# Kernel tuning notes

Hardware: AMD Instinct MI355X
Metric: run time of the kernel (lower is better)

The kernel has to match this reference:

```python
import jax, jax.numpy as jnp
import numpy as np

N_NODES = 50000
N_EDGES = 800000
DIM_IN, DIM_H, DIM_OUT = 256, 128, 64  # hidden widths: 256 -> 128 -> 64, sage1 out = 2*DIM_H


def sage_conv(x, src, dst, Wl, bl, Wr):
    # PyG SAGEConv (mean aggr): out = lin_l(mean over incoming x_src) + lin_r(x)
    n = x.shape[0]
    agg = jax.ops.segment_sum(x[src], dst, num_segments=n)  # [N, F]
    deg = jax.ops.segment_sum(jnp.ones((src.shape[0],), x.dtype), dst, num_segments=n)
    mean = agg / jnp.maximum(deg, 1.0)[:, None]
    return mean @ Wl + bl + x @ Wr


def setup_inputs() -> dict:
    key = jax.random.key(0)
    ks = jax.random.split(key, 12)
    def lin(k, fan_in, fan_out):
        bound = 1.0 / np.sqrt(fan_in)
        return jax.random.uniform(k, (fan_in, fan_out), jnp.float32, -bound, bound)
    h1 = 2 * DIM_H  # 256
    return {
        "x": jax.random.normal(ks[0], (N_NODES, DIM_IN), jnp.float32),
        "edge_index": jax.random.randint(ks[1], (2, N_EDGES), 0, N_NODES, jnp.int64),
        "W1l": lin(ks[2], DIM_IN, h1), "b1": jnp.zeros((h1,), jnp.float32), "W1r": lin(ks[3], DIM_IN, h1),
        "W2l": lin(ks[4], h1, DIM_H), "b2": jnp.zeros((DIM_H,), jnp.float32), "W2r": lin(ks[5], h1, DIM_H),
        "W3l": lin(ks[6], DIM_H, DIM_OUT), "b3": jnp.zeros((DIM_OUT,), jnp.float32), "W3r": lin(ks[7], DIM_H, DIM_OUT),
    }


def reference(x, edge_index, W1l, b1, W1r, W2l, b2, W2r, W3l, b3, W3r):
    src, dst = edge_index[0], edge_index[1]
    h = jax.nn.relu(sage_conv(x, src, dst, W1l, b1, W1r))
    # dropout disabled (training=False)
    h = jax.nn.relu(sage_conv(h, src, dst, W2l, b2, W2r))
    h = sage_conv(h, src, dst, W3l, b3, W3r)
    return (h, jax.nn.log_softmax(h, axis=1))
```

## Files before the change

kernel.cpp:

```cpp
#include <hip/hip_runtime.h>
#include <hip/hip_bf16.h>

#define N_NODES 50000
#define N_EDGES 800000
#define MP 50048
#define NB 98
#define BSH 9
#define CAP 10240

typedef unsigned short ushort_t;
typedef unsigned int uint_t;
typedef __attribute__((ext_vector_type(8))) __bf16 bf16x8;
typedef __attribute__((ext_vector_type(4))) float f32x4;
typedef __attribute__((ext_vector_type(2))) float f32x2;

__device__ __forceinline__ float bf2f(uint_t u) {
    union { uint_t i; float f; } v; v.i = u << 16; return v.f;
}
__device__ __forceinline__ ushort_t f2bf(float f) {
    union { float f; uint_t i; } v; v.f = f;
    uint_t u = v.i;
    return (ushort_t)((u + 0x7FFFu + ((u >> 16) & 1u)) >> 16);
}
__device__ __forceinline__ void accf8(float* a, uint2 d) {
    f32x2 p;
    p = __builtin_amdgcn_cvt_pk_f32_fp8(d.x, false); a[0] += p.x; a[1] += p.y;
    p = __builtin_amdgcn_cvt_pk_f32_fp8(d.x, true);  a[2] += p.x; a[3] += p.y;
    p = __builtin_amdgcn_cvt_pk_f32_fp8(d.y, false); a[4] += p.x; a[5] += p.y;
    p = __builtin_amdgcn_cvt_pk_f32_fp8(d.y, true);  a[6] += p.x; a[7] += p.y;
}
__device__ __forceinline__ uint_t pk_hi(float a, float b) {
    return __builtin_amdgcn_perm(__float_as_uint(b), __float_as_uint(a), 0x07060302);
}

__device__ __forceinline__ void pack_one(const float* Wl, const float* Wr,
                                         ushort_t* P, int K, int F, int t) {
    int NOUT = 2 * F;
    int lane = t & 63;
    int frag = t >> 6;
    int nct = NOUT / 16;
    int ct = frag % nct;
    int kt = frag / nct;
    int col = ct * 16 + (lane & 15);
    const float* W = (col < F) ? Wl : Wr;
    int c = (col < F) ? col : col - F;
    int k0 = kt * 32 + (lane >> 4) * 8;
    uint_t w[4];
    #pragma unroll
    for (int p = 0; p < 4; ++p) {
        ushort_t lo = f2bf(W[(size_t)(k0 + 2 * p) * F + c]);
        ushort_t hi = f2bf(W[(size_t)(k0 + 2 * p + 1) * F + c]);
        w[p] = (uint_t)lo | ((uint_t)hi << 16);
    }
    *(reinterpret_cast<uint4*>(P) + t) = make_uint4(w[0], w[1], w[2], w[3]);
}

__global__ void pack_all_k(const float* __restrict__ W1l, const float* __restrict__ W1r,
                           const float* __restrict__ W2l, const float* __restrict__ W2r,
                           const float* __restrict__ W3l, const float* __restrict__ W3r,
                           ushort_t* __restrict__ pB1, ushort_t* __restrict__ pB2,
                           ushort_t* __restrict__ pB3, int* __restrict__ bcur) {
    int tid = blockIdx.x * 256 + threadIdx.x;
    if (tid < 16384)       pack_one(W1l, W1r, pB1, 256, 256, tid);
    else if (tid < 24576)  pack_one(W2l, W2r, pB2, 256, 128, tid - 16384);
    else if (tid < 26624)  pack_one(W3l, W3r, pB3, 128, 64, tid - 24576);
    else {
        int z = tid - 26624;
        if (z < NB) bcur[z] = z * CAP;
    }
}

__global__ __launch_bounds__(256) void binA_k(const int* __restrict__ src,
                                              const int* __restrict__ dst,
                                              int* __restrict__ bcur,
                                              uint_t* __restrict__ ebuf, int E) {
    __shared__ int cnt[NB];
    __shared__ int base[NB];
    int t = threadIdx.x;
    if (t < NB) cnt[t] = 0;
    __syncthreads();
    int myE = blockIdx.x * 2048 + t * 8;
    uint_t pk[8];
    int bk[8];
    int nval = 0;
    if (myE + 8 <= E) {
        int4 d0 = *reinterpret_cast<const int4*>(dst + myE);
        int4 d1 = *reinterpret_cast<const int4*>(dst + myE + 4);
        int4 s0 = *reinterpret_cast<const int4*>(src + myE);
        int4 s1 = *reinterpret_cast<const int4*>(src + myE + 4);
        int dd[8] = {d0.x, d0.y, d0.z, d0.w, d1.x, d1.y, d1.z, d1.w};
        int ss[8] = {s0.x, s0.y, s0.z, s0.w, s1.x, s1.y, s1.z, s1.w};
        nval = 8;
        #pragma unroll
        for (int i = 0; i < 8; ++i) {
            pk[i] = ((uint_t)dd[i] << 16) | (uint_t)ss[i];
            bk[i] = dd[i] >> BSH;
            atomicAdd(&cnt[bk[i]], 1);
        }
    } else {
        for (int e = myE; e < E && nval < 8; ++e) {
            int d = dst[e];
            pk[nval] = ((uint_t)d << 16) | (uint_t)src[e];
            bk[nval] = d >> BSH;
            atomicAdd(&cnt[bk[nval]], 1);
            ++nval;
        }
    }
    __syncthreads();
    if (t < NB) {
        int c = cnt[t];
        base[t] = c ? atomicAdd(&bcur[t], c) : 0;
        cnt[t] = 0;
    }
    __syncthreads();
    for (int i = 0; i < nval; ++i) {
        int r = atomicAdd(&cnt[bk[i]], 1);
        ebuf[base[bk[i]] + r] = pk[i];
    }
}

__global__ void scanB_k(const int* __restrict__ bcur, int* __restrict__ sOffs) {
    __shared__ int s[128];
    int t = threadIdx.x;
    int c = (t < NB) ? (bcur[t] - t * CAP) : 0;
    s[t] = c;
    __syncthreads();
    #pragma unroll
    for (int d = 1; d < 128; d <<= 1) {
        int v = (t >= d) ? s[t - d] : 0;
        __syncthreads();
        s[t] += v;
        __syncthreads();
    }
    if (t < NB) sOffs[t] = s[t] - c;
}

__global__ __launch_bounds__(256) void binB2_k(const uint_t* __restrict__ ebuf,
                                               const int* __restrict__ bcur,
                                               const int* __restrict__ sOffs,
                                               int* __restrict__ offs,
                                               ushort_t* __restrict__ csrc) {
    __shared__ uint_t eLDS[CAP];
    __shared__ int lhist[512];
    __shared__ int lpre[512];
    __shared__ ushort_t lsrc[CAP];
    int b = blockIdx.x;
    int t = threadIdx.x;
    int n0 = b << BSH;
    int cntE = bcur[b] - b * CAP;
    int obase = sOffs[b];

    for (int i = t; i < 512; i += 256) lhist[i] = 0;
    __syncthreads();
    for (int i = t; i < cntE; i += 256) {
        uint_t pk = ebuf[b * CAP + i];
        eLDS[i] = pk;
        atomicAdd(&lhist[(int)(pk >> 16) - n0], 1);
    }
    __syncthreads();
    int h0 = lhist[2 * t], h1 = lhist[2 * t + 1];
    int pairv = h0 + h1;
    lpre[t] = pairv;
    __syncthreads();
    #pragma unroll
    for (int d = 1; d < 256; d <<= 1) {
        int v = (t >= d) ? lpre[t - d] : 0;
        __syncthreads();
        lpre[t] += v;
        __syncthreads();
    }
    int excl = lpre[t] - pairv;
    __syncthreads();
    lpre[2 * t] = excl;
    lpre[2 * t + 1] = excl + h0;
    __syncthreads();
    for (int i = t; i < 512; i += 256) {
        int node = n0 + i;
        if (node < N_NODES) offs[node] = obase + lpre[i];
    }
    if (b == NB - 1 && t == 0) offs[N_NODES] = N_EDGES;
    for (int i = t; i < 512; i += 256) lhist[i] = lpre[i];
    __syncthreads();
    for (int i = t; i < cntE; i += 256) {
        uint_t pk = eLDS[i];
        int p = atomicAdd(&lhist[(int)(pk >> 16) - n0], 1);
        lsrc[p] = (ushort_t)(pk & 0xffffu);
    }
    __syncthreads();
    for (int i = t; i < cntE; i += 256) csrc[obase + i] = lsrc[i];
}

template <int K, int NOUT, int NCB, int PF, bool F32A, int BPG>
__global__ __launch_bounds__(256, 2) void gemm_k(
    const void* __restrict__ Av, const ushort_t* __restrict__ Bp,
    unsigned char* __restrict__ Pout, ushort_t* __restrict__ Rout, int nvalid) {
    constexpr int KT = K / 32;
    constexpr int CTW = NCB / 64;
    constexpr int NCG = NOUT / NCB;
    constexpr int RS = NOUT - PF;
    constexpr int PADE = K + 8;
    constexpr int NTILES = MP / 32;
    constexpr int NWR = K / 64;
    __shared__ ushort_t Atile[32 * PADE];

    int cg = (NCG > 1) ? ((int)blockIdx.x % NCG) : 0;
    int bid = (NCG > 1) ? ((int)blockIdx.x / NCG) : (int)blockIdx.x;
    int wave = threadIdx.x >> 6;
    int lane = threadIdx.x & 63;
    int ct0 = cg * (NCB / 16) + wave * CTW;

    bf16x8 breg[KT][CTW];
    #pragma unroll
    for (int kt = 0; kt < KT; ++kt)
        #pragma unroll
        for (int ct = 0; ct < CTW; ++ct)
            breg[kt][ct] = *reinterpret_cast<const bf16x8*>(
                Bp + ((size_t)(kt * (NOUT / 16) + ct0 + ct) * 64 + lane) * 8);

    int arowoff = lane & 15;
    int r0 = (lane >> 4) * 4;
    int srow = threadIdx.x >> 3;
    int sel = (threadIdx.x & 7) * (K / 8);

    for (int t = bid; t < NTILES; t += BPG) {
        int rowBase = t * 32;
        __syncthreads();
        {
            int grow = min(rowBase + srow, nvalid - 1);
            ushort_t* dst = &Atile[srow * PADE + sel];
            if (F32A) {
                const float* A = (const float*)Av + (size_t)grow * K + sel;
                #pragma unroll
                for (int i = 0; i < NWR; ++i) {
                    float4 f0 = *reinterpret_cast<const float4*>(A + i * 8);
                    float4 f1 = *reinterpret_cast<const float4*>(A + i * 8 + 4);
                    uint4 w;
                    w.x = pk_hi(f0.x, f0.y);
                    w.y = pk_hi(f0.z, f0.w);
                    w.z = pk_hi(f1.x, f1.y);
                    w.w = pk_hi(f1.z, f1.w);
                    *reinterpret_cast<uint4*>(dst + i * 8) = w;
                }
            } else {
                const ushort_t* A = (const ushort_t*)Av + (size_t)grow * K + sel;
                #pragma unroll
                for (int i = 0; i < NWR; ++i)
                    *reinterpret_cast<uint4*>(dst + i * 8) =
                        *reinterpret_cast<const uint4*>(A + i * 8);
            }
        }
        __syncthreads();

        f32x4 acc[2][CTW];
        #pragma unroll
        for (int r = 0; r < 2; ++r)
            #pragma unroll
            for (int c = 0; c < CTW; ++c) acc[r][c] = (f32x4){0.f, 0.f, 0.f, 0.f};

        const ushort_t* A0 = &Atile[arowoff * PADE + (lane >> 4) * 8];
        #pragma unroll
        for (int kt = 0; kt < KT; ++kt) {
            bf16x8 x0 = *reinterpret_cast<const bf16x8*>(A0 + kt * 32);
            bf16x8 x1 = *reinterpret_cast<const bf16x8*>(A0 + 16 * PADE + kt * 32);
            #pragma unroll
            for (int ct = 0; ct < CTW; ++ct) {
                acc[0][ct] = __builtin_amdgcn_mfma_f32_16x16x32_bf16(breg[kt][ct], x0, acc[0][ct], 0, 0, 0);
                acc[1][ct] = __builtin_amdgcn_mfma_f32_16x16x32_bf16(breg[kt][ct], x1, acc[1][ct], 0, 0, 0);
            }
        }

        #pragma unroll
        for (int r = 0; r < 2; ++r) {
            int xrow = rowBase + r * 16 + arowoff;
            #pragma unroll
            for (int ct = 0; ct < CTW; ++ct) {
                int wc = (ct0 + ct) * 16 + r0;
                f32x4 v = acc[r][ct];
                if (PF > 0 && wc < PF) {
                    uint_t u = __builtin_amdgcn_cvt_pk_fp8_f32(v[0], v[1], 0u, false);
                    u = __builtin_amdgcn_cvt_pk_fp8_f32(v[2], v[3], u, true);
                    *reinterpret_cast<uint_t*>(Pout + (size_t)xrow * PF + wc) = u;
                } else {
                    uint2 w;
                    w.x = (uint_t)f2bf(v[0]) | ((uint_t)f2bf(v[1]) << 16);
                    w.y = (uint_t)f2bf(v[2]) | ((uint_t)f2bf(v[3]) << 16);
                    *reinterpret_cast<uint2*>(Rout + (size_t)xrow * RS + (wc - PF)) = w;
                }
            }
        }
    }
}

template <int F, bool FINAL>
__global__ __launch_bounds__(256) void aggP8_k(
    const unsigned char* __restrict__ P, const int* __restrict__ offs,
    const ushort_t* __restrict__ csrc, const ushort_t* __restrict__ R,
    const float* __restrict__ bias, ushort_t* __restrict__ H,
    float* __restrict__ hout, float* __restrict__ lout, int n) {
    constexpr int LPG = F / 8;
    constexpr int G = 64 / LPG;
    constexpr int U = (G >= 4) ? 1 : (4 / G);
    constexpr int ST = G * U;
    int wid = (blockIdx.x * 256 + threadIdx.x) >> 6;
    int lane = threadIdx.x & 63;
    int g = lane / LPG;
    int sub = lane & (LPG - 1);
    int colbase = sub * 8;
    int n0 = 2 * wid, n1 = 2 * wid + 1;
    if (n0 >= n) return;
    bool has1 = (n1 < n);
    int b0 = offs[n0], end0 = offs[n0 + 1];
    int b1 = has1 ? offs[n1] : 0, end1 = has1 ? offs[n1 + 1] : 0;

    float a0[8] = {0,0,0,0,0,0,0,0};
    float a1[8] = {0,0,0,0,0,0,0,0};
    int e0 = b0, e1 = b1;
    const unsigned char* Pc = P + colbase;

    while (e0 + ST <= end0 && e1 + ST <= end1) {
        uint2 d0[U], d1[U];
        #pragma unroll
        for (int u = 0; u < U; ++u) {
            int s = csrc[e0 + g + u * G];
            d0[u] = *reinterpret_cast<const uint2*>(Pc + (size_t)s * F);
        }
        #pragma unroll
        for (int u = 0; u < U; ++u) {
            int s = csrc[e1 + g + u * G];
            d1[u] = *reinterpret_cast<const uint2*>(Pc + (size_t)s * F);
        }
        #pragma unroll
        for (int u = 0; u < U; ++u) { accf8(a0, d0[u]); accf8(a1, d1[u]); }
        e0 += ST; e1 += ST;
    }
    while (e0 + ST <= end0) {
        uint2 d[U];
        #pragma unroll
        for (int u = 0; u < U; ++u) {
            int s = csrc[e0 + g + u * G];
            d[u] = *reinterpret_cast<const uint2*>(Pc + (size_t)s * F);
        }
        #pragma unroll
        for (int u = 0; u < U; ++u) accf8(a0, d[u]);
        e0 += ST;
    }
    for (int e = e0 + g; e < end0; e += G) {
        int s = csrc[e];
        uint2 d = *reinterpret_cast<const uint2*>(Pc + (size_t)s * F);
        accf8(a0, d);
    }
    while (e1 + ST <= end1) {
        uint2 d[U];
        #pragma unroll
        for (int u = 0; u < U; ++u) {
            int s = csrc[e1 + g + u * G];
            d[u] = *reinterpret_cast<const uint2*>(Pc + (size_t)s * F);
        }
        #pragma unroll
        for (int u = 0; u < U; ++u) accf8(a1, d[u]);
        e1 += ST;
    }
    for (int e = e1 + g; e < end1; e += G) {
        int s = csrc[e];
        uint2 d = *reinterpret_cast<const uint2*>(Pc + (size_t)s * F);
        accf8(a1, d);
    }

    #pragma unroll
    for (int off = LPG; off < 64; off <<= 1) {
        #pragma unroll
        for (int i = 0; i < 8; ++i) {
            a0[i] += __shfl_xor(a0[i], off);
            a1[i] += __shfl_xor(a1[i], off);
        }
    }

    float inv0 = 1.f / fmaxf((float)(end0 - b0), 1.f);
    float inv1 = 1.f / fmaxf((float)(end1 - b1), 1.f);

    #pragma unroll
    for (int j = 0; j < 2; ++j) {
        if (j && !has1) break;
        int node = j ? n1 : n0;
        float* a = j ? a1 : a0;
        float inv = j ? inv1 : inv0;
        uint4 rr = *reinterpret_cast<const uint4*>(R + (size_t)node * F + colbase);
        float r[8];
        r[0] = bf2f(rr.x & 0xffff); r[1] = bf2f(rr.x >> 16);
        r[2] = bf2f(rr.y & 0xffff); r[3] = bf2f(rr.y >> 16);
        r[4] = bf2f(rr.z & 0xffff); r[5] = bf2f(rr.z >> 16);
        r[6] = bf2f(rr.w & 0xffff); r[7] = bf2f(rr.w >> 16);
        float4 bA = *reinterpret_cast<const float4*>(bias + colbase);
        float4 bB = *reinterpret_cast<const float4*>(bias + colbase + 4);
        float bv[8] = {bA.x, bA.y, bA.z, bA.w, bB.x, bB.y, bB.z, bB.w};
        float v[8];
        #pragma unroll
        for (int i = 0; i < 8; ++i) v[i] = a[i] * inv + r[i] + bv[i];

        if constexpr (!FINAL) {
            if (lane < LPG) {
                uint_t w[4];
                #pragma unroll
                for (int p = 0; p < 4; ++p) {
                    float v0 = fmaxf(v[2 * p], 0.f);
                    float v1 = fmaxf(v[2 * p + 1], 0.f);
                    w[p] = (uint_t)f2bf(v0) | ((uint_t)f2bf(v1) << 16);
                }
                *reinterpret_cast<uint4*>(H + (size_t)node * F + colbase) =
                    make_uint4(w[0], w[1], w[2], w[3]);
            }
        } else {
            float m = v[0];
            #pragma unroll
            for (int i = 1; i < 8; ++i) m = fmaxf(m, v[i]);
            #pragma unroll
            for (int off = 1; off < LPG; off <<= 1) m = fmaxf(m, __shfl_xor(m, off));
            float s = 0.f;
            #pragma unroll
            for (int i = 0; i < 8; ++i) s += expf(v[i] - m);
            #pragma unroll
            for (int off = 1; off < LPG; off <<= 1) s += __shfl_xor(s, off);
            float ls = m + logf(s);
            if (lane < LPG) {
                float* ho = hout + (size_t)node * 64 + colbase;
                float* lo = lout + (size_t)node * 64 + colbase;
                *reinterpret_cast<float4*>(ho) = make_float4(v[0], v[1], v[2], v[3]);
                *reinterpret_cast<float4*>(ho + 4) = make_float4(v[4], v[5], v[6], v[7]);
                *reinterpret_cast<float4*>(lo) =
                    make_float4(v[0] - ls, v[1] - ls, v[2] - ls, v[3] - ls);
                *reinterpret_cast<float4*>(lo + 4) =
                    make_float4(v[4] - ls, v[5] - ls, v[6] - ls, v[7] - ls);
            }
        }
    }
}

extern "C" void kernel_launch(void* const* d_in, const int* in_sizes, int n_in,
                              void* d_out, int out_size, void* d_ws, size_t ws_size,
                              hipStream_t stream) {
    const float* x   = (const float*)d_in[0];
    const int*   ei  = (const int*)d_in[1];
    const float* W1l = (const float*)d_in[2];
    const float* b1  = (const float*)d_in[3];
    const float* W1r = (const float*)d_in[4];
    const float* W2l = (const float*)d_in[5];
    const float* b2  = (const float*)d_in[6];
    const float* W2r = (const float*)d_in[7];
    const float* W3l = (const float*)d_in[8];
    const float* b3  = (const float*)d_in[9];
    const float* W3r = (const float*)d_in[10];
    const int* esrc = ei;
    const int* edst = ei + N_EDGES;

    char* ws = (char*)d_ws;
    size_t off = 0;
    auto alloc = [&](size_t b) { void* p = ws + off; off = (off + b + 255) & ~(size_t)255; return p; };
    unsigned char* P1 = (unsigned char*)alloc((size_t)MP * 256);
    ushort_t* R1 = (ushort_t*)alloc((size_t)MP * 256 * 2);
    ushort_t* H1 = (ushort_t*)alloc((size_t)MP * 256 * 2);
    ushort_t* H2 = (ushort_t*)alloc((size_t)MP * 128 * 2);
    int* offs = (int*)alloc((N_NODES + 1) * 4);
    int* bcur = (int*)alloc(NB * 4);
    int* sOffs = (int*)alloc(NB * 4);
    ushort_t* csrc = (ushort_t*)alloc(N_EDGES * 2);
    uint_t* ebuf = (uint_t*)alloc((size_t)NB * CAP * 4);
    ushort_t* pB1 = (ushort_t*)alloc(256 * 512 * 2);
    ushort_t* pB2 = (ushort_t*)alloc(256 * 256 * 2);
    ushort_t* pB3 = (ushort_t*)alloc(128 * 128 * 2);

    unsigned char* P2 = P1;
    ushort_t* R2 = R1;
    unsigned char* P3 = P1;
    ushort_t* R3 = R1;

    pack_all_k<<<(26624 + NB + 255) / 256, 256, 0, stream>>>(
        W1l, W1r, W2l, W2r, W3l, W3r, pB1, pB2, pB3, bcur);

    binA_k<<<(N_EDGES + 2047) / 2048, 256, 0, stream>>>(esrc, edst, bcur, ebuf, N_EDGES);
    scanB_k<<<1, 128, 0, stream>>>(bcur, sOffs);
    binB2_k<<<NB, 256, 0, stream>>>(ebuf, bcur, sOffs, offs, csrc);

    constexpr int BPG = 512;
    int aggGrid = ((N_NODES + 1) / 2 + 3) / 4;
    float* hout = (float*)d_out;
    float* lout = hout + (size_t)N_NODES * 64;

    gemm_k<256, 512, 256, 256, true, BPG><<<2 * BPG, 256, 0, stream>>>(x, pB1, P1, R1, N_NODES);
    aggP8_k<256, false><<<aggGrid, 256, 0, stream>>>(
        P1, offs, csrc, R1, b1, H1, nullptr, nullptr, N_NODES);
    gemm_k<256, 256, 256, 128, false, BPG><<<BPG, 256, 0, stream>>>(H1, pB2, P2, R2, N_NODES);
    aggP8_k<128, false><<<aggGrid, 256, 0, stream>>>(
        P2, offs, csrc, R2, b2, H2, nullptr, nullptr, N_NODES);
    gemm_k<128, 128, 128, 64, false, BPG><<<BPG, 256, 0, stream>>>(H2, pB3, P3, R3, N_NODES);
    aggP8_k<64, true><<<aggGrid, 256, 0, stream>>>(
        P3, offs, csrc, R3, b3, nullptr, hout, lout, N_NODES);
}
```

Measured before the change: 191.3 us.

## Merge preprocessing kernels and co-schedule CSR build with first-layer GEMM

Weight packing and edge binning now run in a single launch. The bucket scan and CSR build run as extra blocks inside the first GEMM launch, so graph preprocessing overlaps the x-projection. bcur is zeroed with a memset, and binA adds t*CAP when computing write positions. The GEMMs drop the persistent grid-stride loop and launch one block per 32-row tile. This cuts the launch count from nine to six, but every CSR block repeats the bucket scan, and one-block-per-tile re-loads the B fragments into registers in every block.

Result: slower. 200.0 us (+4.5%).

```diff
diff --git a/kernel.cpp b/kernel.cpp
--- a/kernel.cpp
+++ b/kernel.cpp
@@ -55,31 +55,31 @@
     *(reinterpret_cast<uint4*>(P) + t) = make_uint4(w[0], w[1], w[2], w[3]);
 }
 
-__global__ void pack_all_k(const float* __restrict__ W1l, const float* __restrict__ W1r,
-                           const float* __restrict__ W2l, const float* __restrict__ W2r,
-                           const float* __restrict__ W3l, const float* __restrict__ W3r,
-                           ushort_t* __restrict__ pB1, ushort_t* __restrict__ pB2,
-                           ushort_t* __restrict__ pB3, int* __restrict__ bcur) {
-    int tid = blockIdx.x * 256 + threadIdx.x;
-    if (tid < 16384)       pack_one(W1l, W1r, pB1, 256, 256, tid);
-    else if (tid < 24576)  pack_one(W2l, W2r, pB2, 256, 128, tid - 16384);
-    else if (tid < 26624)  pack_one(W3l, W3r, pB3, 128, 64, tid - 24576);
-    else {
-        int z = tid - 26624;
-        if (z < NB) bcur[z] = z * CAP;
-    }
-}
-
-__global__ __launch_bounds__(256) void binA_k(const int* __restrict__ src,
-                                              const int* __restrict__ dst,
-                                              int* __restrict__ bcur,
-                                              uint_t* __restrict__ ebuf, int E) {
+#define PACK_BLOCKS 104
+#define BINA_BLOCKS ((N_EDGES + 2047) / 2048)
+
+__global__ __launch_bounds__(256) void prep_k(
+    const float* __restrict__ W1l, const float* __restrict__ W1r,
+    const float* __restrict__ W2l, const float* __restrict__ W2r,
+    const float* __restrict__ W3l, const float* __restrict__ W3r,
+    ushort_t* __restrict__ pB1, ushort_t* __restrict__ pB2,
+    ushort_t* __restrict__ pB3,
+    const int* __restrict__ src, const int* __restrict__ dst,
+    int* __restrict__ bcur, uint_t* __restrict__ ebuf, int E) {
     __shared__ int cnt[NB];
     __shared__ int base[NB];
     int t = threadIdx.x;
+    if ((int)blockIdx.x < PACK_BLOCKS) {
+        int tid = blockIdx.x * 256 + t;
+        if (tid < 16384)       pack_one(W1l, W1r, pB1, 256, 256, tid);
+        else if (tid < 24576)  pack_one(W2l, W2r, pB2, 256, 128, tid - 16384);
+        else if (tid < 26624)  pack_one(W3l, W3r, pB3, 128, 64, tid - 24576);
+        return;
+    }
+    int bb = (int)blockIdx.x - PACK_BLOCKS;
     if (t < NB) cnt[t] = 0;
     __syncthreads();
-    int myE = blockIdx.x * 2048 + t * 8;
+    int myE = bb * 2048 + t * 8;
     uint_t pk[8];
     int bk[8];
     int nval = 0;
@@ -109,7 +109,7 @@
     __syncthreads();
     if (t < NB) {
         int c = cnt[t];
-        base[t] = c ? atomicAdd(&bcur[t], c) : 0;
+        base[t] = c ? (t * CAP + atomicAdd(&bcur[t], c)) : 0;
         cnt[t] = 0;
     }
     __syncthreads();
@@ -119,138 +119,62 @@
     }
 }
 
-__global__ void scanB_k(const int* __restrict__ bcur, int* __restrict__ sOffs) {
-    __shared__ int s[128];
-    int t = threadIdx.x;
-    int c = (t < NB) ? (bcur[t] - t * CAP) : 0;
-    s[t] = c;
-    __syncthreads();
-    #pragma unroll
-    for (int d = 1; d < 128; d <<= 1) {
-        int v = (t >= d) ? s[t - d] : 0;
-        __syncthreads();
-        s[t] += v;
-        __syncthreads();
-    }
-    if (t < NB) sOffs[t] = s[t] - c;
-}
-
-__global__ __launch_bounds__(256) void binB2_k(const uint_t* __restrict__ ebuf,
-                                               const int* __restrict__ bcur,
-                                               const int* __restrict__ sOffs,
-                                               int* __restrict__ offs,
-                                               ushort_t* __restrict__ csrc) {
-    __shared__ uint_t eLDS[CAP];
-    __shared__ int lhist[512];
-    __shared__ int lpre[512];
-    __shared__ ushort_t lsrc[CAP];
-    int b = blockIdx.x;
-    int t = threadIdx.x;
-    int n0 = b << BSH;
-    int cntE = bcur[b] - b * CAP;
-    int obase = sOffs[b];
-
-    for (int i = t; i < 512; i += 256) lhist[i] = 0;
-    __syncthreads();
-    for (int i = t; i < cntE; i += 256) {
-        uint_t pk = ebuf[b * CAP + i];
-        eLDS[i] = pk;
-        atomicAdd(&lhist[(int)(pk >> 16) - n0], 1);
-    }
-    __syncthreads();
-    int h0 = lhist[2 * t], h1 = lhist[2 * t + 1];
-    int pairv = h0 + h1;
-    lpre[t] = pairv;
-    __syncthreads();
-    #pragma unroll
-    for (int d = 1; d < 256; d <<= 1) {
-        int v = (t >= d) ? lpre[t - d] : 0;
-        __syncthreads();
-        lpre[t] += v;
-        __syncthreads();
-    }
-    int excl = lpre[t] - pairv;
-    __syncthreads();
-    lpre[2 * t] = excl;
-    lpre[2 * t + 1] = excl + h0;
-    __syncthreads();
-    for (int i = t; i < 512; i += 256) {
-        int node = n0 + i;
-        if (node < N_NODES) offs[node] = obase + lpre[i];
-    }
-    if (b == NB - 1 && t == 0) offs[N_NODES] = N_EDGES;
-    for (int i = t; i < 512; i += 256) lhist[i] = lpre[i];
-    __syncthreads();
-    for (int i = t; i < cntE; i += 256) {
-        uint_t pk = eLDS[i];
-        int p = atomicAdd(&lhist[(int)(pk >> 16) - n0], 1);
-        lsrc[p] = (ushort_t)(pk & 0xffffu);
-    }
-    __syncthreads();
-    for (int i = t; i < cntE; i += 256) csrc[obase + i] = lsrc[i];
-}
-
-template <int K, int NOUT, int NCB, int PF, bool F32A, int BPG>
-__global__ __launch_bounds__(256, 2) void gemm_k(
-    const void* __restrict__ Av, const ushort_t* __restrict__ Bp,
-    unsigned char* __restrict__ Pout, ushort_t* __restrict__ Rout, int nvalid) {
+#define G1_NCG 2
+#define G1_GRID (G1_NCG * (MP / 32))
+
+__global__ __launch_bounds__(256, 2) void big1_k(
+    const float* __restrict__ x, const ushort_t* __restrict__ Bp,
+    unsigned char* __restrict__ Pout, ushort_t* __restrict__ Rout,
+    const uint_t* __restrict__ ebuf, const int* __restrict__ bcur,
+    int* __restrict__ offs, ushort_t* __restrict__ csrc, int nvalid) {
+    __shared__ char smem[25088];
+    constexpr int K = 256, NOUT = 512, NCB = 256, PF = 256;
     constexpr int KT = K / 32;
     constexpr int CTW = NCB / 64;
-    constexpr int NCG = NOUT / NCB;
     constexpr int RS = NOUT - PF;
     constexpr int PADE = K + 8;
-    constexpr int NTILES = MP / 32;
     constexpr int NWR = K / 64;
-    __shared__ ushort_t Atile[32 * PADE];
-
-    int cg = (NCG > 1) ? ((int)blockIdx.x % NCG) : 0;
-    int bid = (NCG > 1) ? ((int)blockIdx.x / NCG) : (int)blockIdx.x;
-    int wave = threadIdx.x >> 6;
-    int lane = threadIdx.x & 63;
-    int ct0 = cg * (NCB / 16) + wave * CTW;
-
-    bf16x8 breg[KT][CTW];
-    #pragma unroll
-    for (int kt = 0; kt < KT; ++kt)
-        #pragma unroll
-        for (int ct = 0; ct < CTW; ++ct)
-            breg[kt][ct] = *reinterpret_cast<const bf16x8*>(
-                Bp + ((size_t)(kt * (NOUT / 16) + ct0 + ct) * 64 + lane) * 8);
-
-    int arowoff = lane & 15;
-    int r0 = (lane >> 4) * 4;
-    int srow = threadIdx.x >> 3;
-    int sel = (threadIdx.x & 7) * (K / 8);
-
-    for (int t = bid; t < NTILES; t += BPG) {
-        int rowBase = t * 32;
-        __syncthreads();
+
+    int t = threadIdx.x;
+    if ((int)blockIdx.x < G1_GRID) {
+        ushort_t* Atile = reinterpret_cast<ushort_t*>(smem);
+        int cg = (int)blockIdx.x % G1_NCG;
+        int tile = (int)blockIdx.x / G1_NCG;
+        int wave = t >> 6;
+        int lane = t & 63;
+        int ct0 = cg * (NCB / 16) + wave * CTW;
+
+        bf16x8 breg[KT][CTW];
+        #pragma unroll
+        for (int kt = 0; kt < KT; ++kt)
+            #pragma unroll
+            for (int ct = 0; ct < CTW; ++ct)
+                breg[kt][ct] = *reinterpret_cast<const bf16x8*>(
+                    Bp + ((size_t)(kt * (NOUT / 16) + ct0 + ct) * 64 + lane) * 8);
+
+        int rowBase = tile * 32;
         {
+            int srow = t >> 3;
+            int sel = (t & 7) * (K / 8);
             int grow = min(rowBase + srow, nvalid - 1);
             ushort_t* dst = &Atile[srow * PADE + sel];
-            if (F32A) {
-                const float* A = (const float*)Av + (size_t)grow * K + sel;
-                #pragma unroll
-                for (int i = 0; i < NWR; ++i) {
-                    float4 f0 = *reinterpret_cast<const float4*>(A + i * 8);
-                    float4 f1 = *reinterpret_cast<const float4*>(A + i * 8 + 4);
-                    uint4 w;
-                    w.x = pk_hi(f0.x, f0.y);
-                    w.y = pk_hi(f0.z, f0.w);
-                    w.z = pk_hi(f1.x, f1.y);
-                    w.w = pk_hi(f1.z, f1.w);
-                    *reinterpret_cast<uint4*>(dst + i * 8) = w;
-                }
-            } else {
-                const ushort_t* A = (const ushort_t*)Av + (size_t)grow * K + sel;
-                #pragma unroll
-                for (int i = 0; i < NWR; ++i)
-                    *reinterpret_cast<uint4*>(dst + i * 8) =
-                        *reinterpret_cast<const uint4*>(A + i * 8);
+            const float* A = x + (size_t)grow * K + sel;
+            #pragma unroll
+            for (int i = 0; i < NWR; ++i) {
+                float4 f0 = *reinterpret_cast<const float4*>(A + i * 8);
+                float4 f1 = *reinterpret_cast<const float4*>(A + i * 8 + 4);
+                uint4 w;
+                w.x = pk_hi(f0.x, f0.y);
+                w.y = pk_hi(f0.z, f0.w);
+                w.z = pk_hi(f1.x, f1.y);
+                w.w = pk_hi(f1.z, f1.w);
+                *reinterpret_cast<uint4*>(dst + i * 8) = w;
             }
         }
         __syncthreads();
 
+        int arowoff = lane & 15;
+        int r0 = (lane >> 4) * 4;
         f32x4 acc[2][CTW];
         #pragma unroll
         for (int r = 0; r < 2; ++r)
@@ -276,7 +200,7 @@
             for (int ct = 0; ct < CTW; ++ct) {
                 int wc = (ct0 + ct) * 16 + r0;
                 f32x4 v = acc[r][ct];
-                if (PF > 0 && wc < PF) {
+                if (wc < PF) {
                     uint_t u = __builtin_amdgcn_cvt_pk_fp8_f32(v[0], v[1], 0u, false);
                     u = __builtin_amdgcn_cvt_pk_fp8_f32(v[2], v[3], u, true);
                     *reinterpret_cast<uint_t*>(Pout + (size_t)xrow * PF + wc) = u;
@@ -286,6 +210,142 @@
                     w.y = (uint_t)f2bf(v[2]) | ((uint_t)f2bf(v[3]) << 16);
                     *reinterpret_cast<uint2*>(Rout + (size_t)xrow * RS + (wc - PF)) = w;
                 }
+            }
+        }
+        return;
+    }
+
+    int b = (int)blockIdx.x - G1_GRID;
+    int* scnt = reinterpret_cast<int*>(smem);
+    int* lhist = reinterpret_cast<int*>(smem + 512);
+    int* lpre = reinterpret_cast<int*>(smem + 2560);
+    ushort_t* lsrc = reinterpret_cast<ushort_t*>(smem + 4608);
+    int n0 = b << BSH;
+
+    int c0 = (t < 128) ? ((t < NB) ? bcur[t] : 0) : 0;
+    if (t < 128) scnt[t] = c0;
+    __syncthreads();
+    for (int d = 1; d < 128; d <<= 1) {
+        int v = (t < 128 && t >= d) ? scnt[t - d] : 0;
+        __syncthreads();
+        if (t < 128) scnt[t] += v;
+        __syncthreads();
+    }
+    int obase = (b > 0) ? scnt[b - 1] : 0;
+    int cntE = bcur[b];
+    __syncthreads();
+
+    for (int i = t; i < 512; i += 256) lhist[i] = 0;
+    __syncthreads();
+    for (int i = t; i < cntE; i += 256)
+        atomicAdd(&lhist[(int)(ebuf[b * CAP + i] >> 16) - n0], 1);
+    __syncthreads();
+    int h0 = lhist[2 * t], h1 = lhist[2 * t + 1];
+    int pairv = h0 + h1;
+    lpre[t] = pairv;
+    __syncthreads();
+    #pragma unroll
+    for (int d = 1; d < 256; d <<= 1) {
+        int v = (t >= d) ? lpre[t - d] : 0;
+        __syncthreads();
+        lpre[t] += v;
+        __syncthreads();
+    }
+    int excl = lpre[t] - pairv;
+    __syncthreads();
+    lpre[2 * t] = excl;
+    lpre[2 * t + 1] = excl + h0;
+    __syncthreads();
+    for (int i = t; i < 512; i += 256) {
+        int node = n0 + i;
+        if (node < N_NODES) offs[node] = obase + lpre[i];
+    }
+    if (b == NB - 1 && t == 0) offs[N_NODES] = N_EDGES;
+    for (int i = t; i < 512; i += 256) lhist[i] = lpre[i];
+    __syncthreads();
+    for (int i = t; i < cntE; i += 256) {
+        uint_t pk = ebuf[b * CAP + i];
+        int p = atomicAdd(&lhist[(int)(pk >> 16) - n0], 1);
+        lsrc[p] = (ushort_t)(pk & 0xffffu);
+    }
+    __syncthreads();
+    for (int i = t; i < cntE; i += 256) csrc[obase + i] = lsrc[i];
+}
+
+template <int K, int NOUT, int NCB, int PF>
+__global__ __launch_bounds__(256, 2) void gemm_k(
+    const ushort_t* __restrict__ Av, const ushort_t* __restrict__ Bp,
+    unsigned char* __restrict__ Pout, ushort_t* __restrict__ Rout, int nvalid) {
+    constexpr int KT = K / 32;
+    constexpr int CTW = NCB / 64;
+    constexpr int RS = NOUT - PF;
+    constexpr int PADE = K + 8;
+    constexpr int NWR = K / 64;
+    __shared__ ushort_t Atile[32 * PADE];
+
+    int tile = (int)blockIdx.x;
+    int wave = threadIdx.x >> 6;
+    int lane = threadIdx.x & 63;
+    int ct0 = wave * CTW;
+
+    bf16x8 breg[KT][CTW];
+    #pragma unroll
+    for (int kt = 0; kt < KT; ++kt)
+        #pragma unroll
+        for (int ct = 0; ct < CTW; ++ct)
+            breg[kt][ct] = *reinterpret_cast<const bf16x8*>(
+                Bp + ((size_t)(kt * (NOUT / 16) + ct0 + ct) * 64 + lane) * 8);
+
+    int rowBase = tile * 32;
+    {
+        int srow = threadIdx.x >> 3;
+        int sel = (threadIdx.x & 7) * (K / 8);
+        int grow = min(rowBase + srow, nvalid - 1);
+        ushort_t* dst = &Atile[srow * PADE + sel];
+        const ushort_t* A = Av + (size_t)grow * K + sel;
+        #pragma unroll
+        for (int i = 0; i < NWR; ++i)
+            *reinterpret_cast<uint4*>(dst + i * 8) =
+                *reinterpret_cast<const uint4*>(A + i * 8);
+    }
+    __syncthreads();
+
+    int arowoff = lane & 15;
+    int r0 = (lane >> 4) * 4;
+    f32x4 acc[2][CTW];
+    #pragma unroll
+    for (int r = 0; r < 2; ++r)
+        #pragma unroll
+        for (int c = 0; c < CTW; ++c) acc[r][c] = (f32x4){0.f, 0.f, 0.f, 0.f};
+
+    const ushort_t* A0 = &Atile[arowoff * PADE + (lane >> 4) * 8];
+    #pragma unroll
+    for (int kt = 0; kt < KT; ++kt) {
+        bf16x8 x0 = *reinterpret_cast<const bf16x8*>(A0 + kt * 32);
+        bf16x8 x1 = *reinterpret_cast<const bf16x8*>(A0 + 16 * PADE + kt * 32);
+        #pragma unroll
+        for (int ct = 0; ct < CTW; ++ct) {
+            acc[0][ct] = __builtin_amdgcn_mfma_f32_16x16x32_bf16(breg[kt][ct], x0, acc[0][ct], 0, 0, 0);
+            acc[1][ct] = __builtin_amdgcn_mfma_f32_16x16x32_bf16(breg[kt][ct], x1, acc[1][ct], 0, 0, 0);
+        }
+    }
+
+    #pragma unroll
+    for (int r = 0; r < 2; ++r) {
+        int xrow = rowBase + r * 16 + arowoff;
+        #pragma unroll
+        for (int ct = 0; ct < CTW; ++ct) {
+            int wc = (ct0 + ct) * 16 + r0;
+            f32x4 v = acc[r][ct];
+            if (wc < PF) {
+                uint_t u = __builtin_amdgcn_cvt_pk_fp8_f32(v[0], v[1], 0u, false);
+                u = __builtin_amdgcn_cvt_pk_fp8_f32(v[2], v[3], u, true);
+                *reinterpret_cast<uint_t*>(Pout + (size_t)xrow * PF + wc) = u;
+            } else {
+                uint2 w;
+                w.x = (uint_t)f2bf(v[0]) | ((uint_t)f2bf(v[1]) << 16);
+                w.y = (uint_t)f2bf(v[2]) | ((uint_t)f2bf(v[3]) << 16);
+                *reinterpret_cast<uint2*>(Rout + (size_t)xrow * RS + (wc - PF)) = w;
             }
         }
     }
@@ -461,7 +521,6 @@
     ushort_t* H2 = (ushort_t*)alloc((size_t)MP * 128 * 2);
     int* offs = (int*)alloc((N_NODES + 1) * 4);
     int* bcur = (int*)alloc(NB * 4);
-    int* sOffs = (int*)alloc(NB * 4);
     ushort_t* csrc = (ushort_t*)alloc(N_EDGES * 2);
     uint_t* ebuf = (uint_t*)alloc((size_t)NB * CAP * 4);
     ushort_t* pB1 = (ushort_t*)alloc(256 * 512 * 2);
@@ -473,25 +532,23 @@
     unsigned char* P3 = P1;
     ushort_t* R3 = R1;
 
-    pack_all_k<<<(26624 + NB + 255) / 256, 256, 0, stream>>>(
-        W1l, W1r, W2l, W2r, W3l, W3r, pB1, pB2, pB3, bcur);
-
-    binA_k<<<(N_EDGES + 2047) / 2048, 256, 0, stream>>>(esrc, edst, bcur, ebuf, N_EDGES);
-    scanB_k<<<1, 128, 0, stream>>>(bcur, sOffs);
-    binB2_k<<<NB, 256, 0, stream>>>(ebuf, bcur, sOffs, offs, csrc);
-
-    constexpr int BPG = 512;
+    hipMemsetAsync(bcur, 0, NB * 4, stream);
+
+    prep_k<<<PACK_BLOCKS + BINA_BLOCKS, 256, 0, stream>>>(
+        W1l, W1r, W2l, W2r, W3l, W3r, pB1, pB2, pB3, esrc, edst, bcur, ebuf, N_EDGES);
+
     int aggGrid = ((N_NODES + 1) / 2 + 3) / 4;
     float* hout = (float*)d_out;
     float* lout = hout + (size_t)N_NODES * 64;
 
-    gemm_k<256, 512, 256, 256, true, BPG><<<2 * BPG, 256, 0, stream>>>(x, pB1, P1, R1, N_NODES);
+    big1_k<<<G1_GRID + NB, 256, 0, stream>>>(
+        x, pB1, P1, R1, ebuf, bcur, offs, csrc, N_NODES);
     aggP8_k<256, false><<<aggGrid, 256, 0, stream>>>(
         P1, offs, csrc, R1, b1, H1, nullptr, nullptr, N_NODES);
-    gemm_k<256, 256, 256, 128, false, BPG><<<BPG, 256, 0, stream>>>(H1, pB2, P2, R2, N_NODES);
+    gemm_k<256, 256, 256, 128><<<MP / 32, 256, 0, stream>>>(H1, pB2, P2, R2, N_NODES);
     aggP8_k<128, false><<<aggGrid, 256, 0, stream>>>(
         P2, offs, csrc, R2, b2, H2, nullptr, nullptr, N_NODES);
-    gemm_k<128, 128, 128, 64, false, BPG><<<BPG, 256, 0, stream>>>(H2, pB3, P3, R3, N_NODES);
+    gemm_k<128, 128, 128, 64><<<MP / 32, 256, 0, stream>>>(H2, pB3, P3, R3, N_NODES);
     aggP8_k<64, true><<<aggGrid, 256, 0, stream>>>(
         P3, offs, csrc, R3, b3, nullptr, hout, lout, N_NODES);
 }
```

## Merge weight packing and edge binning kernels, fold bucket scan into binB2

Applied to the files above, without the earlier changes.

Weight packing and the first edge-binning pass now run as one kernel, with the first blocks doing packing and the rest binning. The bucket cursors become zero-based counts, reset by a memset. The separate single-block scan kernel is removed: each binB2 block recomputes the prefix sum over bucket counts itself. The LDS staging copy of the edge buffer is dropped and the buffer is re-read from global memory instead. The aim is to cut kernel launches and serial dependencies in the preprocessing chain, at the cost of a redundant scan in every block and a second global read.

New measurement: 193.6 us. Within noise of the previous version (+1.2%).

```diff
diff --git a/kernel.cpp b/kernel.cpp
--- a/kernel.cpp
+++ b/kernel.cpp
@@ -55,31 +55,31 @@
     *(reinterpret_cast<uint4*>(P) + t) = make_uint4(w[0], w[1], w[2], w[3]);
 }
 
-__global__ void pack_all_k(const float* __restrict__ W1l, const float* __restrict__ W1r,
-                           const float* __restrict__ W2l, const float* __restrict__ W2r,
-                           const float* __restrict__ W3l, const float* __restrict__ W3r,
-                           ushort_t* __restrict__ pB1, ushort_t* __restrict__ pB2,
-                           ushort_t* __restrict__ pB3, int* __restrict__ bcur) {
-    int tid = blockIdx.x * 256 + threadIdx.x;
-    if (tid < 16384)       pack_one(W1l, W1r, pB1, 256, 256, tid);
-    else if (tid < 24576)  pack_one(W2l, W2r, pB2, 256, 128, tid - 16384);
-    else if (tid < 26624)  pack_one(W3l, W3r, pB3, 128, 64, tid - 24576);
-    else {
-        int z = tid - 26624;
-        if (z < NB) bcur[z] = z * CAP;
-    }
-}
-
-__global__ __launch_bounds__(256) void binA_k(const int* __restrict__ src,
-                                              const int* __restrict__ dst,
-                                              int* __restrict__ bcur,
-                                              uint_t* __restrict__ ebuf, int E) {
+#define PACK_BLOCKS 104
+#define BINA_BLOCKS ((N_EDGES + 2047) / 2048)
+
+__global__ __launch_bounds__(256) void prep_k(
+    const float* __restrict__ W1l, const float* __restrict__ W1r,
+    const float* __restrict__ W2l, const float* __restrict__ W2r,
+    const float* __restrict__ W3l, const float* __restrict__ W3r,
+    ushort_t* __restrict__ pB1, ushort_t* __restrict__ pB2,
+    ushort_t* __restrict__ pB3,
+    const int* __restrict__ src, const int* __restrict__ dst,
+    int* __restrict__ bcur, uint_t* __restrict__ ebuf, int E) {
     __shared__ int cnt[NB];
     __shared__ int base[NB];
     int t = threadIdx.x;
+    if ((int)blockIdx.x < PACK_BLOCKS) {
+        int tid = blockIdx.x * 256 + t;
+        if (tid < 16384)       pack_one(W1l, W1r, pB1, 256, 256, tid);
+        else if (tid < 24576)  pack_one(W2l, W2r, pB2, 256, 128, tid - 16384);
+        else if (tid < 26624)  pack_one(W3l, W3r, pB3, 128, 64, tid - 24576);
+        return;
+    }
+    int bb = (int)blockIdx.x - PACK_BLOCKS;
     if (t < NB) cnt[t] = 0;
     __syncthreads();
-    int myE = blockIdx.x * 2048 + t * 8;
+    int myE = bb * 2048 + t * 8;
     uint_t pk[8];
     int bk[8];
     int nval = 0;
@@ -109,7 +109,7 @@
     __syncthreads();
     if (t < NB) {
         int c = cnt[t];
-        base[t] = c ? atomicAdd(&bcur[t], c) : 0;
+        base[t] = c ? (t * CAP + atomicAdd(&bcur[t], c)) : 0;
         cnt[t] = 0;
     }
     __syncthreads();
@@ -119,44 +119,35 @@
     }
 }
 
-__global__ void scanB_k(const int* __restrict__ bcur, int* __restrict__ sOffs) {
-    __shared__ int s[128];
-    int t = threadIdx.x;
-    int c = (t < NB) ? (bcur[t] - t * CAP) : 0;
-    s[t] = c;
-    __syncthreads();
-    #pragma unroll
-    for (int d = 1; d < 128; d <<= 1) {
-        int v = (t >= d) ? s[t - d] : 0;
-        __syncthreads();
-        s[t] += v;
-        __syncthreads();
-    }
-    if (t < NB) sOffs[t] = s[t] - c;
-}
-
 __global__ __launch_bounds__(256) void binB2_k(const uint_t* __restrict__ ebuf,
                                                const int* __restrict__ bcur,
-                                               const int* __restrict__ sOffs,
                                                int* __restrict__ offs,
                                                ushort_t* __restrict__ csrc) {
-    __shared__ uint_t eLDS[CAP];
+    __shared__ int scnt[128];
     __shared__ int lhist[512];
     __shared__ int lpre[512];
     __shared__ ushort_t lsrc[CAP];
     int b = blockIdx.x;
     int t = threadIdx.x;
     int n0 = b << BSH;
-    int cntE = bcur[b] - b * CAP;
-    int obase = sOffs[b];
+
+    int c0 = (t < 128) ? ((t < NB) ? bcur[t] : 0) : 0;
+    if (t < 128) scnt[t] = c0;
+    __syncthreads();
+    for (int d = 1; d < 128; d <<= 1) {
+        int v = (t < 128 && t >= d) ? scnt[t - d] : 0;
+        __syncthreads();
+        if (t < 128) scnt[t] += v;
+        __syncthreads();
+    }
+    int obase = (b > 0) ? scnt[b - 1] : 0;
+    int cntE = bcur[b];
+    __syncthreads();
 
     for (int i = t; i < 512; i += 256) lhist[i] = 0;
     __syncthreads();
-    for (int i = t; i < cntE; i += 256) {
-        uint_t pk = ebuf[b * CAP + i];
-        eLDS[i] = pk;
-        atomicAdd(&lhist[(int)(pk >> 16) - n0], 1);
-    }
+    for (int i = t; i < cntE; i += 256)
+        atomicAdd(&lhist[(int)(ebuf[b * CAP + i] >> 16) - n0], 1);
     __syncthreads();
     int h0 = lhist[2 * t], h1 = lhist[2 * t + 1];
     int pairv = h0 + h1;
@@ -182,7 +173,7 @@
     for (int i = t; i < 512; i += 256) lhist[i] = lpre[i];
     __syncthreads();
     for (int i = t; i < cntE; i += 256) {
-        uint_t pk = eLDS[i];
+        uint_t pk = ebuf[b * CAP + i];
         int p = atomicAdd(&lhist[(int)(pk >> 16) - n0], 1);
         lsrc[p] = (ushort_t)(pk & 0xffffu);
     }
@@ -461,7 +452,6 @@
     ushort_t* H2 = (ushort_t*)alloc((size_t)MP * 128 * 2);
     int* offs = (int*)alloc((N_NODES + 1) * 4);
     int* bcur = (int*)alloc(NB * 4);
-    int* sOffs = (int*)alloc(NB * 4);
     ushort_t* csrc = (ushort_t*)alloc(N_EDGES * 2);
     uint_t* ebuf = (uint_t*)alloc((size_t)NB * CAP * 4);
     ushort_t* pB1 = (ushort_t*)alloc(256 * 512 * 2);
@@ -473,12 +463,11 @@
     unsigned char* P3 = P1;
     ushort_t* R3 = R1;
 
-    pack_all_k<<<(26624 + NB + 255) / 256, 256, 0, stream>>>(
-        W1l, W1r, W2l, W2r, W3l, W3r, pB1, pB2, pB3, bcur);
-
-    binA_k<<<(N_EDGES + 2047) / 2048, 256, 0, stream>>>(esrc, edst, bcur, ebuf, N_EDGES);
-    scanB_k<<<1, 128, 0, stream>>>(bcur, sOffs);
-    binB2_k<<<NB, 256, 0, stream>>>(ebuf, bcur, sOffs, offs, csrc);
+    hipMemsetAsync(bcur, 0, NB * 4, stream);
+
+    prep_k<<<PACK_BLOCKS + BINA_BLOCKS, 256, 0, stream>>>(
+        W1l, W1r, W2l, W2r, W3l, W3r, pB1, pB2, pB3, esrc, edst, bcur, ebuf, N_EDGES);
+    binB2_k<<<NB, 256, 0, stream>>>(ebuf, bcur, offs, csrc);
 
     constexpr int BPG = 512;
     int aggGrid = ((N_NODES + 1) / 2 + 3) / 4;
```
